# Performance work log

Hardware: AMD Instinct MI355X
Metric: run time of the kernel (lower is better)

## Reference

```python
import jax, jax.numpy as jnp
import numpy as np

RADIUS = 0.15
NSAMPLE = 128
NPOINT = 128
EPS = 1e-5  # BatchNorm eps (eval mode, running_mean=0, running_var=1)


def _bn(x, g, b):
    shape = (1, -1) + (1,) * (x.ndim - 2)
    return x * (g / jnp.sqrt(1.0 + EPS)).reshape(shape) + b.reshape(shape)


def _fps(x, npoint):
    # farthest point sampling; x: (Bk, N, 3) -> (Bk, npoint) int32
    Bn, N, _ = x.shape

    def step(carry, _):
        dist, far = carry
        c = jnp.take_along_axis(x, far[:, None, None], 1)  # (Bk,1,3)
        d = jnp.sum((x - c) ** 2, -1)
        dist = jnp.minimum(dist, d)
        return (dist, jnp.argmax(dist, -1).astype(jnp.int32)), far

    init = (jnp.full((Bn, N), 1e10, x.dtype), jnp.zeros((Bn,), jnp.int32))
    _, idxs = jax.lax.scan(step, init, None, length=npoint)
    return idxs.T  # (Bk, npoint)


def _sa_module(x, f, mlp):
    # PointnetSAModuleVotes: FPS -> ball query -> group (use_xyz, normalize_xyz)
    # -> shared MLP (conv2d 1x1 + BN + ReLU) -> max over nsample.
    Bk, M, _ = x.shape
    fps_idx = _fps(x, NPOINT)
    new_xyz = jnp.take_along_axis(x, fps_idx[..., None], 1)  # (Bk,np,3)
    d2 = jnp.sum((new_xyz[:, :, None, :] - x[:, None, :, :]) ** 2, -1)  # (Bk,np,M)
    cand = jnp.where(d2 < RADIUS ** 2, jnp.arange(M)[None, None, :], M)
    cand = jnp.sort(cand, -1)[..., :NSAMPLE]  # first nsample in-radius indices
    first = cand[..., :1]
    first = jnp.where(first == M, 0, first)
    idx = jnp.where(cand == M, first, cand)  # (Bk,np,ns), pad with first valid
    gx = jnp.take_along_axis(x, idx.reshape(Bk, -1)[..., None], 1).reshape(Bk, NPOINT, NSAMPLE, 3)
    gxn = (gx - new_xyz[:, :, None, :]) / RADIUS  # normalize_xyz=True
    gf = jnp.take_along_axis(f[:, :, None, :], idx[:, None, :, :], 3)  # (Bk,C,np,ns)
    h = jnp.concatenate([gxn.transpose(0, 3, 1, 2), gf], 1)  # (Bk, C+3, np, ns)
    for (w, b, g, be) in mlp:
        h = jax.nn.relu(_bn(jnp.einsum('oc,bcps->bops', w, h) + b[None, :, None, None], g, be))
    return new_xyz, h.max(-1)  # (Bk,np,3), (Bk,128,np)


def setup_inputs() -> dict:
    key = jax.random.key(0)
    ks = iter(jax.random.split(key, 40))
    B, M, K, C = 2, 1024, 19, 256
    inp = {}
    inp['xyz'] = jax.random.normal(next(ks), (B, M, K, 3), jnp.float32)
    inp['features'] = jax.random.normal(next(ks), (B, C, K, M), jnp.float32)

    def conv_p(prefix, cin, cout):
        inp[prefix + '_w'] = jax.random.normal(next(ks), (cout, cin), jnp.float32) * (1.0 / np.sqrt(cin))
        inp[prefix + '_b'] = jax.random.normal(next(ks), (cout,), jnp.float32) * 0.02
        inp[prefix + '_g'] = 1.0 + 0.1 * jax.random.normal(next(ks), (cout,), jnp.float32)
        inp[prefix + '_be'] = 0.02 * jax.random.normal(next(ks), (cout,), jnp.float32)

    conv_p('m1', C + 3, 128)  # use_xyz -> 259 in-channels
    conv_p('m2', 128, 128)
    conv_p('m3', 128, 128)
    conv_p('c1', 128, 128)
    conv_p('c2', 128, 128)
    inp['op_w'] = jax.random.normal(next(ks), (K, 5, 128), jnp.float32) * (1.0 / np.sqrt(128))
    inp['op_b'] = jax.random.normal(next(ks), (K, 5), jnp.float32) * 0.02
    return inp


def reference(xyz, features, m1_w, m1_b, m1_g, m1_be, m2_w, m2_b, m2_g, m2_be,
              m3_w, m3_b, m3_g, m3_be, c1_w, c1_b, c1_g, c1_be,
              c2_w, c2_b, c2_g, c2_be, op_w, op_b):
    B, M, K, _ = xyz.shape
    C = features.shape[1]
    # fold vote_factor k into the batch dim (all per-k SA/conv weights are shared)
    x = xyz.transpose(0, 2, 1, 3).reshape(B * K, M, 3)
    f = features.transpose(0, 2, 1, 3).reshape(B * K, C, M)
    mlp = [(m1_w, m1_b, m1_g, m1_be), (m2_w, m2_b, m2_g, m2_be), (m3_w, m3_b, m3_g, m3_be)]
    new_xyz, feat = _sa_module(x, f, mlp)
    net = jax.nn.relu(_bn(jnp.einsum('oc,bcp->bop', c1_w, feat) + c1_b[None, :, None], c1_g, c1_be))
    net = jax.nn.relu(_bn(jnp.einsum('oc,bcp->bop', c2_w, net) + c2_b[None, :, None], c2_g, c2_be))
    net = net.reshape(B, K, 128, NPOINT)
    # per-k output conv (conv_op ModuleList), 128 -> 2+3
    out = jnp.einsum('koc,bkcp->bkop', op_w, net) + op_b[None, :, :, None]
    net_t = out.transpose(0, 1, 3, 2)  # (B,K,np,5)
    agg_xyz = new_xyz.reshape(B, K, NPOINT, 3)
    center = agg_xyz + net_t[..., 2:5]  # decode_scores_
    scores = jnp.concatenate([net_t[..., :2], center], -1)  # obj(2) + center(3)
    return scores, agg_xyz, feat.reshape(B, K, 128, NPOINT)
```

## Files before the change

### kernel.cpp

```cpp
#include <hip/hip_runtime.h>
#include <math.h>

#define NBK   38

#define OFF_XC    0u
#define OFF_NXYZ  466944u
#define OFF_BIDX  525312u
#define OFF_W1F   3015680u
#define OFF_PREP  22938624u
#define OFF_WF    22955008u
#define OFF_CNT   23348224u

#define OUT_AGG   24320
#define OUT_FEAT  38912

typedef short bf16x8 __attribute__((ext_vector_type(8)));
typedef float f32x4  __attribute__((ext_vector_type(4)));
typedef int   v4i    __attribute__((ext_vector_type(4)));
typedef int   v2i    __attribute__((ext_vector_type(2)));

__device__ __forceinline__ float dist2f(float a0, float a1, float a2,
                                        float b0, float b1, float b2) {
#pragma clang fp contract(off)
  float d0 = a0 - b0;
  float d1 = a1 - b1;
  float d2 = a2 - b2;
  return d0 * d0 + d1 * d1 + d2 * d2;
}

__device__ __forceinline__ void split2rn(float v, unsigned& sh, unsigned& sm) {
  unsigned u = __float_as_uint(v);
  unsigned rh = (u + 0x7fffu + ((u >> 16) & 1u)) & 0xffff0000u;
  sh = rh >> 16;
  float r1 = v - __uint_as_float(rh);
  unsigned u1 = __float_as_uint(r1);
  unsigned rm = (u1 + 0x7fffu + ((u1 >> 16) & 1u)) & 0xffff0000u;
  sm = rm >> 16;
}

template<int CTRL, int RMASK>
__device__ __forceinline__ float fmax_dpp(float x) {
  int o = __builtin_amdgcn_update_dpp(__float_as_int(x), __float_as_int(x),
                                      CTRL, RMASK, 0xf, false);
  return fmaxf(x, __int_as_float(o));
}
template<int CTRL, int RMASK>
__device__ __forceinline__ unsigned umax_dpp(unsigned x) {
  unsigned o = (unsigned)__builtin_amdgcn_update_dpp((int)x, (int)x,
                                                     CTRL, RMASK, 0xf, false);
  return o > x ? o : x;
}
__device__ __forceinline__ float wave_fmax(float x) {
  x = fmax_dpp<0x111, 0xf>(x);
  x = fmax_dpp<0x112, 0xf>(x);
  x = fmax_dpp<0x114, 0xf>(x);
  x = fmax_dpp<0x118, 0xf>(x);
  x = fmax_dpp<0x142, 0xa>(x);
  x = fmax_dpp<0x143, 0xc>(x);
  return __int_as_float(__builtin_amdgcn_readlane(__float_as_int(x), 63));
}
__device__ __forceinline__ unsigned wave_umax(unsigned x) {
  x = umax_dpp<0x111, 0xf>(x);
  x = umax_dpp<0x112, 0xf>(x);
  x = umax_dpp<0x114, 0xf>(x);
  x = umax_dpp<0x118, 0xf>(x);
  x = umax_dpp<0x142, 0xa>(x);
  x = umax_dpp<0x143, 0xc>(x);
  return (unsigned)__builtin_amdgcn_readlane((int)x, 63);
}

__global__ __launch_bounds__(256, 2) void front_kernel(
    const float* __restrict__ xyz, const float* __restrict__ feats,
    const float* __restrict__ m1w, const float* __restrict__ m1b,
    const float* __restrict__ m1g, const float* __restrict__ m1be,
    const float* __restrict__ m2w, const float* __restrict__ m2b,
    const float* __restrict__ m2g, const float* __restrict__ m2be,
    const float* __restrict__ m3w, const float* __restrict__ m3b,
    const float* __restrict__ m3g, const float* __restrict__ m3be,
    const float* __restrict__ c1w, const float* __restrict__ c1b,
    const float* __restrict__ c1g, const float* __restrict__ c1be,
    const float* __restrict__ c2w, const float* __restrict__ c2b,
    const float* __restrict__ c2g, const float* __restrict__ c2be,
    float* __restrict__ xc, float* __restrict__ nxyz, float* __restrict__ agg,
    int* __restrict__ bidx, int* __restrict__ counts,
    float* __restrict__ W1f, short* __restrict__ Wf, float* __restrict__ prep)
{
  __shared__ __align__(16) char smem[32768];
  int bid = blockIdx.x, t = threadIdx.x;
  int wave = t >> 6, lane = t & 63;

  if (bid < NBK) {
    int bk = bid;
    int b = bk / 19, k = bk % 19;
    float* sx0 = (float*)smem;
    float* sx1 = sx0 + 1024;
    float* sx2 = sx1 + 1024;
    float* scen = sx2 + 1024;
    int* slot = (int*)(scen + 384);

    float x0[4], x1[4], x2[4], dist[4];
#pragma unroll
    for (int j = 0; j < 4; ++j) {
      int i = j * 256 + t;
      const float* src = xyz + ((size_t)((b * 1024 + i) * 19 + k)) * 3;
      x0[j] = src[0]; x1[j] = src[1]; x2[j] = src[2];
      sx0[i] = x0[j]; sx1[i] = x1[j]; sx2[i] = x2[j];
      xc[(bk * 3 + 0) * 1024 + i] = x0[j];
      xc[(bk * 3 + 1) * 1024 + i] = x1[j];
      xc[(bk * 3 + 2) * 1024 + i] = x2[j];
      dist[j] = 1e10f;
    }
    if (t == 0) {
#pragma unroll
      for (int w = 0; w < 4; ++w) {
        int* s = slot + w * 8;
        s[0] = 0; s[1] = 1023;
        s[2] = __float_as_int(x0[0]);
        s[3] = __float_as_int(x1[0]);
        s[4] = __float_as_int(x2[0]);
      }
    }
    __syncthreads();

    for (int it = 0; it < 128; ++it) {
      int pi = it & 1;
      const int* sl = slot + pi * 32;
      v4i s0 = *(const v4i*)(sl + 0);  int z0 = sl[4];
      v4i s1 = *(const v4i*)(sl + 8);  int z1 = sl[12];
      v4i s2 = *(const v4i*)(sl + 16); int z2 = sl[20];
      v4i s3 = *(const v4i*)(sl + 24); int z3 = sl[28];
      unsigned long long k0 = ((unsigned long long)(unsigned)s0.x << 32) | (unsigned)s0.y;
      unsigned long long k1 = ((unsigned long long)(unsigned)s1.x << 32) | (unsigned)s1.y;
      unsigned long long k2 = ((unsigned long long)(unsigned)s2.x << 32) | (unsigned)s2.y;
      unsigned long long k3 = ((unsigned long long)(unsigned)s3.x << 32) | (unsigned)s3.y;
      if (k1 > k0) { k0 = k1; s0 = s1; z0 = z1; }
      if (k3 > k2) { k2 = k3; s2 = s3; z2 = z3; }
      if (k2 > k0) { k0 = k2; s0 = s2; z0 = z2; }
      float c0 = __int_as_float(s0.z);
      float c1 = __int_as_float(s0.w);
      float c2 = __int_as_float(z0);
      if (t < 3) scen[it * 3 + t] = (t == 0) ? c0 : ((t == 1) ? c1 : c2);
      float dbest = -1.f; int ibest = 0;
#pragma unroll
      for (int j = 0; j < 4; ++j) {
        float d = dist2f(x0[j], x1[j], x2[j], c0, c1, c2);
        float dj = fminf(dist[j], d);
        dist[j] = dj;
        if (dj > dbest) { dbest = dj; ibest = j * 256 + t; }
      }
      float dmax = wave_fmax(dbest);
      unsigned cand = (dbest == dmax) ? (unsigned)(1023 - ibest) : 0u;
      unsigned key = wave_umax(cand);
      if (dbest == dmax && (unsigned)(1023 - ibest) == key) {
        int j = ibest >> 8;
        float wx = (j == 0) ? x0[0] : (j == 1) ? x0[1] : (j == 2) ? x0[2] : x0[3];
        float wy = (j == 0) ? x1[0] : (j == 1) ? x1[1] : (j == 2) ? x1[2] : x1[3];
        float wz = (j == 0) ? x2[0] : (j == 1) ? x2[1] : (j == 2) ? x2[2] : x2[3];
        int* s = slot + (pi ^ 1) * 32 + wave * 8;
        s[0] = __float_as_int(dmax);
        s[1] = (int)key;
        s[2] = __float_as_int(wx);
        s[3] = __float_as_int(wy);
        s[4] = __float_as_int(wz);
      }
      __syncthreads();
    }

    for (int e = t; e < 384; e += 256) {
      float v = scen[e];
      nxyz[bk * 384 + e] = v;
      agg[bk * 384 + e]  = v;
    }

    for (int p = wave * 32; p < wave * 32 + 32; ++p) {
      float c0 = scen[p * 3 + 0], c1 = scen[p * 3 + 1], c2 = scen[p * 3 + 2];
      int* outp = bidx + ((size_t)(bk * 128 + p)) * 128;
      int count = 0, first = 0;
      bool got = false;
      for (int ch = 0; ch < 16 && count < 128; ++ch) {
        int m = (ch << 6) + lane;
        float d = dist2f(sx0[m], sx1[m], sx2[m], c0, c1, c2);
        bool flag = d < 0.0225f;
        unsigned long long mask = __ballot(flag);
        if (!got && mask) { first = (ch << 6) + __builtin_ctzll(mask); got = true; }
        int pos = count + (int)__popcll(mask & ((1ull << lane) - 1ull));
        if (flag && pos < 128) outp[pos] = m;
        count += (int)__popcll(mask);
      }
      for (int j = count + lane; j < 128; j += 64) outp[j] = first;
      if (lane == 0) counts[bk * 128 + p] = count > 128 ? 128 : count;
    }
    return;
  }

  if (bid < 342) {
    short* ffrag = (short*)smem;
    int blk = bid - NBK;
    int bk = blk >> 3, m0 = (blk & 7) << 7;
    int b = bk / 19, k = bk % 19;
    int quad = lane >> 4, nl = lane & 15;
    int mloc = t & 127, chalf = t >> 7;
    int st_w = mloc >> 4, sl_w = mloc & 15;
    const float* fbase = feats + ((size_t)(b * 4864 + k)) * 1024 + m0 + mloc;
    const short* WA = Wf + 65536;

    f32x4 acc[2][8];
#pragma unroll
    for (int oi = 0; oi < 2; ++oi)
#pragma unroll
      for (int st = 0; st < 8; ++st) acc[oi][st] = (f32x4){0.f, 0.f, 0.f, 0.f};

    for (int ch = 0; ch < 4; ++ch) {
      int cbase = ch * 64 + chalf * 32;
#pragma unroll
      for (int g = 0; g < 4; ++g) {
        float v[8];
#pragma unroll
        for (int j = 0; j < 8; ++j)
          v[j] = fbase[(size_t)(cbase + g * 8 + j) * 19456];
        unsigned sh[8], sm[8];
#pragma unroll
        for (int j = 0; j < 8; ++j) split2rn(v[j], sh[j], sm[j]);
        int base = chalf * 4096 + st_w * 512 + (g * 16 + sl_w) * 8;
        v4i ph = {(int)(sh[0] | (sh[1] << 16)), (int)(sh[2] | (sh[3] << 16)),
                  (int)(sh[4] | (sh[5] << 16)), (int)(sh[6] | (sh[7] << 16))};
        *(v4i*)&ffrag[base] = ph;
        v4i pm = {(int)(sm[0] | (sm[1] << 16)), (int)(sm[2] | (sm[3] << 16)),
                  (int)(sm[4] | (sm[5] << 16)), (int)(sm[6] | (sm[7] << 16))};
        *(v4i*)&ffrag[base + 8192] = pm;
      }
      __syncthreads();
#pragma unroll
      for (int kkl = 0; kkl < 2; ++kkl) {
        int kk = ch * 2 + kkl;
        bf16x8 a[2][2];
#pragma unroll
        for (int oi = 0; oi < 2; ++oi) {
          int o_row = (wave * 2 + oi) * 16 + nl;
          const float* wsrc = m1w + o_row * 259 + 3 + kk * 32 + quad * 8;
          float wv[8];
#pragma unroll
          for (int j = 0; j < 8; ++j) wv[j] = wsrc[j];
          unsigned sh[8], sm[8];
#pragma unroll
          for (int j = 0; j < 8; ++j) split2rn(wv[j], sh[j], sm[j]);
          short ah[8], am[8];
#pragma unroll
          for (int j = 0; j < 8; ++j) { ah[j] = (short)sh[j]; am[j] = (short)sm[j]; }
          a[oi][0] = (bf16x8){ah[0], ah[1], ah[2], ah[3], ah[4], ah[5], ah[6], ah[7]};
          a[oi][1] = (bf16x8){am[0], am[1], am[2], am[3], am[4], am[5], am[6], am[7]};
        }
#pragma unroll
        for (int st = 0; st < 8; ++st) {
          const short* hb = ffrag + kkl * 4096 + st * 512 + lane * 8;
          bf16x8 b0 = *(const bf16x8*)hb;
          bf16x8 b1 = *(const bf16x8*)(hb + 8192);
#pragma unroll
          for (int oi = 0; oi < 2; ++oi) {
            f32x4 c = acc[oi][st];
            c = __builtin_amdgcn_mfma_f32_16x16x32_bf16(a[oi][1], b0, c, 0, 0, 0);
            c = __builtin_amdgcn_mfma_f32_16x16x32_bf16(a[oi][0], b1, c, 0, 0, 0);
            c = __builtin_amdgcn_mfma_f32_16x16x32_bf16(a[oi][0], b0, c, 0, 0, 0);
            acc[oi][st] = c;
          }
        }
      }
      __syncthreads();
    }
    (void)WA;
    float inv = 1.0f / sqrtf(1.0f + 1e-5f);
#pragma unroll
    for (int oi = 0; oi < 2; ++oi) {
      int o0 = (wave * 2 + oi) * 16 + quad * 4;
      float4 bb = *(const float4*)&m1b[o0];
      float4 gg = *(const float4*)&m1g[o0];
#pragma unroll
      for (int st = 0; st < 8; ++st) {
        int m_out = m0 + st * 16 + nl;
        f32x4 cc = acc[oi][st];
        float4 r;
        r.x = (cc[0] + bb.x) * (gg.x * inv);
        r.y = (cc[1] + bb.y) * (gg.y * inv);
        r.z = (cc[2] + bb.z) * (gg.z * inv);
        r.w = (cc[3] + bb.w) * (gg.w * inv);
        *(float4*)&W1f[((size_t)(bk * 1024 + m_out)) * 128 + o0] = r;
      }
    }
    return;
  }

  if (bid < 406) {
    int idx = (bid - 342) * 256 + t;
#pragma unroll
    for (int e = 0; e < 4; ++e) {
      int i = idx * 4 + e;
      if (i < 32768) {
        int c = i & 127, o = (i >> 7) & 127, l = i >> 14;
        float w = (l ? m3w : m2w)[o * 128 + c];
        unsigned sh, sm;
        split2rn(w, sh, sm);
        int ot = o >> 4, mm = o & 15, kk = c >> 5, q = (c & 31) >> 3, j = c & 7;
        int within = (q * 16 + mm) * 8 + j;
        Wf[(((l * 2 + 0) * 4 + kk) * 8 + ot) * 512 + within] = (short)sh;
        Wf[(((l * 2 + 1) * 4 + kk) * 8 + ot) * 512 + within] = (short)sm;
      } else {
        int jdx = i - 32768;
        int o = jdx >> 8, c = jdx & 255;
        float w = m1w[o * 259 + 3 + c];
        unsigned sh, sm;
        split2rn(w, sh, sm);
        int ot = o >> 4, mm = o & 15, kk = c >> 5, q = (c & 31) >> 3, j = c & 7;
        int within = (q * 16 + mm) * 8 + j;
        Wf[65536 + ((kk) * 8 + ot) * 512 + within] = (short)sh;
        Wf[65536 + ((8 + kk) * 8 + ot) * 512 + within] = (short)sm;
      }
    }
    return;
  }

  if (bid < 438) {
    int idx2 = (bid - 406) * 256 + t;
#pragma unroll
    for (int e = 0; e < 4; ++e) {
      int i = idx2 * 4 + e;
      int c = i & 127, o = (i >> 7) & 127, l = i >> 14;
      float w = (l ? c2w : c1w)[o * 128 + c];
      unsigned sh, sm;
      split2rn(w, sh, sm);
      int ot = o >> 4, mm = o & 15, kk = c >> 5, q = (c & 31) >> 3, j = c & 7;
      int within = (q * 16 + mm) * 8 + j;
      Wf[131072 + (((l * 2 + 0) * 4 + kk) * 8 + ot) * 512 + within] = (short)sh;
      Wf[131072 + (((l * 2 + 1) * 4 + kk) * 8 + ot) * 512 + within] = (short)sm;
    }
    return;
  }

  if (t < 128) {
    float inv = 1.0f / sqrtf(1.0f + 1e-5f);
    float a1 = m1g[t] * inv;
    prep[t] = a1;
    float a2 = m2g[t] * inv;  prep[256 + t] = a2;  prep[384 + t] = fmaf(m2b[t], a2, m2be[t]);
    float a3 = m3g[t] * inv;  prep[512 + t] = a3;  prep[640 + t] = fmaf(m3b[t], a3, m3be[t]);
    float ac1 = c1g[t] * inv; prep[768 + t] = ac1; prep[896 + t] = fmaf(c1b[t], ac1, c1be[t]);
    float ac2 = c2g[t] * inv; prep[1024 + t] = ac2; prep[1152 + t] = fmaf(c2b[t], ac2, c2be[t]);
    prep[1280 + 4 * t + 0] = m1w[t * 259 + 0] * a1;
    prep[1280 + 4 * t + 1] = m1w[t * 259 + 1] * a1;
    prep[1280 + 4 * t + 2] = m1w[t * 259 + 2] * a1;
    prep[1280 + 4 * t + 3] = m1be[t];
  }
}

__device__ __forceinline__ void mfma_layer(const short* __restrict__ Wf,
                                           const short* hfrag, int l,
                                           int wave, int lane, int nst_h,
                                           f32x4 acc[2][4])
{
#pragma unroll 1
  for (int kk = 0; kk < 4; ++kk) {
    bf16x8 a[2][2];
#pragma unroll
    for (int oi = 0; oi < 2; ++oi)
#pragma unroll
      for (int sp = 0; sp < 2; ++sp)
        a[oi][sp] = *(const bf16x8*)(Wf + (((l * 2 + sp) * 4 + kk) * 8 + (wave * 2 + oi)) * 512 + lane * 8);
    for (int st = 0; st < nst_h; ++st) {
      const short* hb = hfrag + kk * 2048 + st * 512 + lane * 8;
      bf16x8 b0 = *(const bf16x8*)(hb);
      bf16x8 b1 = *(const bf16x8*)(hb + 8192);
#pragma unroll
      for (int oi = 0; oi < 2; ++oi) {
        f32x4 c = acc[oi][st];
        c = __builtin_amdgcn_mfma_f32_16x16x32_bf16(a[oi][1], b0, c, 0, 0, 0);
        c = __builtin_amdgcn_mfma_f32_16x16x32_bf16(a[oi][0], b1, c, 0, 0, 0);
        c = __builtin_amdgcn_mfma_f32_16x16x32_bf16(a[oi][0], b0, c, 0, 0, 0);
        acc[oi][st] = c;
      }
    }
  }
}

__global__ __launch_bounds__(256, 3) void sa_kernel(
    const float* __restrict__ xc, const float* __restrict__ nxyz,
    const int* __restrict__ bidx, const int* __restrict__ counts,
    const float* __restrict__ W1f, const float* __restrict__ prep,
    const short* __restrict__ Wf, float* __restrict__ feat_out)
{
  __shared__ __align__(16) short hfrag[16384];
  __shared__ float pcs[512];
  __shared__ float sm[32 * 128];
  __shared__ float ccen[12];
  __shared__ int scnt[4];
  int gb = blockIdx.x, bk = gb >> 5, pb = (gb & 31) << 2;
  int t = threadIdx.x;
  int wave = t >> 6, lane = t & 63;
  int quad = lane >> 4, nl = lane & 15;

  pcs[t] = prep[1280 + t];
  pcs[256 + t] = prep[1536 + t];
  if (t < 4) scnt[t] = counts[bk * 128 + pb + t];
  if (t < 12) {
    int bb = t / 3, c = t % 3;
    ccen[t] = nxyz[(bk * 128 + pb + bb) * 3 + c];
  }
  __syncthreads();
  int n0 = (scnt[0] + 15) >> 4, n1 = (scnt[1] + 15) >> 4;
  int n2 = (scnt[2] + 15) >> 4, n3 = (scnt[3] + 15) >> 4;
  int pf1 = n0, pf2 = n0 + n1, pf3 = n0 + n1 + n2, T = n0 + n1 + n2 + n3;

  for (int q0 = 0; q0 < T; q0 += 4) {
    int nst_h = T - q0;
    if (nst_h > 4) nst_h = 4;
    {
      int cg = wave;
      int st = lane >> 4, sl = lane & 15;
      if (st < nst_h) {
        int q = q0 + st;
        int bq = (q >= pf1) + (q >= pf2) + (q >= pf3);
        int tstart = (bq == 0) ? 0 : (bq == 1) ? pf1 : (bq == 2) ? pf2 : pf3;
        int tslot = q - tstart;
        int m = bidx[((size_t)(bk * 128 + pb + bq)) * 128 + tslot * 16 + sl];
        float cen0 = ccen[bq * 3 + 0], cen1 = ccen[bq * 3 + 1], cen2 = ccen[bq * 3 + 2];
        float g0 = (xc[(bk * 3 + 0) * 1024 + m] - cen0) * (1.0f / 0.15f);
        float g1 = (xc[(bk * 3 + 1) * 1024 + m] - cen1) * (1.0f / 0.15f);
        float g2 = (xc[(bk * 3 + 2) * 1024 + m] - cen2) * (1.0f / 0.15f);
        const float4* wrow = (const float4*)(W1f + ((size_t)(bk * 1024 + m)) * 128 + cg * 32);
        const float4* pcp = (const float4*)pcs + cg * 32;
#pragma unroll
        for (int g = 0; g < 4; ++g) {
          float4 wva = wrow[g * 2], wvb = wrow[g * 2 + 1];
          float wv[8] = {wva.x, wva.y, wva.z, wva.w, wvb.x, wvb.y, wvb.z, wvb.w};
          unsigned sh[8], smv[8];
#pragma unroll
          for (int e = 0; e < 8; ++e) {
            float4 pc = pcp[g * 8 + e];
            float hv = fmaxf(wv[e] + pc.x * g0 + pc.y * g1 + pc.z * g2 + pc.w, 0.f);
            split2rn(hv, sh[e], smv[e]);
          }
          int base = (cg * 4 + st) * 512 + (g * 16 + sl) * 8;
          v4i ph = {(int)(sh[0] | (sh[1] << 16)), (int)(sh[2] | (sh[3] << 16)),
                    (int)(sh[4] | (sh[5] << 16)), (int)(sh[6] | (sh[7] << 16))};
          *(v4i*)&hfrag[base] = ph;
          v4i pm = {(int)(smv[0] | (smv[1] << 16)), (int)(smv[2] | (smv[3] << 16)),
                    (int)(smv[4] | (smv[5] << 16)), (int)(smv[6] | (smv[7] << 16))};
          *(v4i*)&hfrag[base + 8192] = pm;
        }
      }
    }
    __syncthreads();

    f32x4 acc[2][4];
#pragma unroll
    for (int oi = 0; oi < 2; ++oi)
#pragma unroll
      for (int st = 0; st < 4; ++st) acc[oi][st] = (f32x4){0.f, 0.f, 0.f, 0.f};
    mfma_layer(Wf, hfrag, 0, wave, lane, nst_h, acc);
    __syncthreads();

#pragma unroll
    for (int oi = 0; oi < 2; ++oi) {
      int o0 = (wave * 2 + oi) * 16 + quad * 4;
      float4 al = *(const float4*)&prep[256 + o0];
      float4 be = *(const float4*)&prep[384 + o0];
      int kk2 = o0 >> 5, g2 = (o0 & 31) >> 3, j0 = o0 & 7;
      for (int st = 0; st < nst_h; ++st) {
        f32x4 cc = acc[oi][st];
        float v0 = fmaxf(fmaf(cc[0], al.x, be.x), 0.f);
        float v1 = fmaxf(fmaf(cc[1], al.y, be.y), 0.f);
        float v2 = fmaxf(fmaf(cc[2], al.z, be.z), 0.f);
        float v3 = fmaxf(fmaf(cc[3], al.w, be.w), 0.f);
        unsigned h0, m0_, h1, m1_, h2, m2_, h3, m3_;
        split2rn(v0, h0, m0_); split2rn(v1, h1, m1_);
        split2rn(v2, h2, m2_); split2rn(v3, h3, m3_);
        int base = (kk2 * 4 + st) * 512 + (g2 * 16 + nl) * 8 + j0;
        v2i w0 = {(int)(h0 | (h1 << 16)), (int)(h2 | (h3 << 16))};
        *(v2i*)&hfrag[base] = w0;
        v2i w1 = {(int)(m0_ | (m1_ << 16)), (int)(m2_ | (m3_ << 16))};
        *(v2i*)&hfrag[base + 8192] = w1;
      }
    }
    __syncthreads();

#pragma unroll
    for (int oi = 0; oi < 2; ++oi)
#pragma unroll
      for (int st = 0; st < 4; ++st) acc[oi][st] = (f32x4){0.f, 0.f, 0.f, 0.f};
    mfma_layer(Wf, hfrag, 1, wave, lane, nst_h, acc);

#pragma unroll
    for (int oi = 0; oi < 2; ++oi) {
      int o0 = (wave * 2 + oi) * 16 + quad * 4;
      float4 al = *(const float4*)&prep[512 + o0];
      float4 be = *(const float4*)&prep[640 + o0];
      for (int st = 0; st < nst_h; ++st) {
        f32x4 cc = acc[oi][st];
        float v[4];
        v[0] = fmaxf(fmaf(cc[0], al.x, be.x), 0.f);
        v[1] = fmaxf(fmaf(cc[1], al.y, be.y), 0.f);
        v[2] = fmaxf(fmaf(cc[2], al.z, be.z), 0.f);
        v[3] = fmaxf(fmaf(cc[3], al.w, be.w), 0.f);
#pragma unroll
        for (int r = 0; r < 4; ++r) {
          float x = v[r];
          x = fmaxf(x, __shfl_xor(x, 1));
          x = fmaxf(x, __shfl_xor(x, 2));
          x = fmaxf(x, __shfl_xor(x, 4));
          x = fmaxf(x, __shfl_xor(x, 8));
          if (nl == 0) sm[(q0 + st) * 128 + o0 + r] = x;
        }
      }
    }
    __syncthreads();
  }

#pragma unroll
  for (int e = t; e < 512; e += 256) {
    int bb = e >> 7, o = e & 127;
    int qs = (bb == 0) ? 0 : (bb == 1) ? pf1 : (bb == 2) ? pf2 : pf3;
    int nq = (bb == 0) ? n0 : (bb == 1) ? n1 : (bb == 2) ? n2 : n3;
    float v = sm[qs * 128 + o];
    for (int q = 1; q < nq; ++q) v = fmaxf(v, sm[(qs + q) * 128 + o]);
    feat_out[(((size_t)bk) << 14) + (o << 7) + pb + bb] = v;
  }
}

__global__ __launch_bounds__(256) void head_kernel(const float* __restrict__ featg,
    const float* __restrict__ prep, const short* __restrict__ Wf,
    const float* __restrict__ nxyz, const float* __restrict__ opw,
    const float* __restrict__ opb, float* __restrict__ scores)
{
  __shared__ __align__(16) short hfrag[16384];
  __shared__ float hplain[128 * 65];
  int bk = blockIdx.x >> 1, p0 = (blockIdx.x & 1) << 6;
  int t = threadIdx.x;
  int wave = t >> 6, lane = t & 63;
  int quad = lane >> 4, nl = lane & 15;
  const short* WC = Wf + 131072;

  {
    int cg = wave;
    int st = lane >> 4, sl = lane & 15;
    const float* fb = featg + (bk << 14) + p0 + lane;
#pragma unroll
    for (int g = 0; g < 4; ++g) {
      float v[8];
#pragma unroll
      for (int e = 0; e < 8; ++e)
        v[e] = fb[(cg * 32 + g * 8 + e) << 7];
      unsigned sh[8], sm[8];
#pragma unroll
      for (int e = 0; e < 8; ++e) split2rn(v[e], sh[e], sm[e]);
      int base = (cg * 4 + st) * 512 + (g * 16 + sl) * 8;
      v4i ph = {(int)(sh[0] | (sh[1] << 16)), (int)(sh[2] | (sh[3] << 16)),
                (int)(sh[4] | (sh[5] << 16)), (int)(sh[6] | (sh[7] << 16))};
      *(v4i*)&hfrag[base] = ph;
      v4i pm = {(int)(sm[0] | (sm[1] << 16)), (int)(sm[2] | (sm[3] << 16)),
                (int)(sm[4] | (sm[5] << 16)), (int)(sm[6] | (sm[7] << 16))};
      *(v4i*)&hfrag[base + 8192] = pm;
    }
  }
  __syncthreads();

  f32x4 acc[2][4];
#pragma unroll
  for (int oi = 0; oi < 2; ++oi)
#pragma unroll
    for (int st = 0; st < 4; ++st) acc[oi][st] = (f32x4){0.f, 0.f, 0.f, 0.f};
  mfma_layer(WC, hfrag, 0, wave, lane, 4, acc);
  __syncthreads();

#pragma unroll
  for (int oi = 0; oi < 2; ++oi) {
    int o0 = (wave * 2 + oi) * 16 + quad * 4;
    float4 al = *(const float4*)&prep[768 + o0];
    float4 be = *(const float4*)&prep[896 + o0];
    int kk2 = o0 >> 5, g2 = (o0 & 31) >> 3, j0 = o0 & 7;
#pragma unroll
    for (int st = 0; st < 4; ++st) {
      f32x4 cc = acc[oi][st];
      float v0 = fmaxf(fmaf(cc[0], al.x, be.x), 0.f);
      float v1 = fmaxf(fmaf(cc[1], al.y, be.y), 0.f);
      float v2 = fmaxf(fmaf(cc[2], al.z, be.z), 0.f);
      float v3 = fmaxf(fmaf(cc[3], al.w, be.w), 0.f);
      unsigned h0, m0_, h1, m1_, h2, m2_, h3, m3_;
      split2rn(v0, h0, m0_); split2rn(v1, h1, m1_);
      split2rn(v2, h2, m2_); split2rn(v3, h3, m3_);
      int base = (kk2 * 4 + st) * 512 + (g2 * 16 + nl) * 8 + j0;
      v2i w0 = {(int)(h0 | (h1 << 16)), (int)(h2 | (h3 << 16))};
      *(v2i*)&hfrag[base] = w0;
      v2i w1 = {(int)(m0_ | (m1_ << 16)), (int)(m2_ | (m3_ << 16))};
      *(v2i*)&hfrag[base + 8192] = w1;
    }
  }
  __syncthreads();

#pragma unroll
  for (int oi = 0; oi < 2; ++oi)
#pragma unroll
    for (int st = 0; st < 4; ++st) acc[oi][st] = (f32x4){0.f, 0.f, 0.f, 0.f};
  mfma_layer(WC, hfrag, 1, wave, lane, 4, acc);

#pragma unroll
  for (int oi = 0; oi < 2; ++oi) {
    int o0 = (wave * 2 + oi) * 16 + quad * 4;
    float4 al = *(const float4*)&prep[1024 + o0];
    float4 be = *(const float4*)&prep[1152 + o0];
#pragma unroll
    for (int st = 0; st < 4; ++st) {
      f32x4 cc = acc[oi][st];
      int p = st * 16 + nl;
      hplain[(o0 + 0) * 65 + p] = fmaxf(fmaf(cc[0], al.x, be.x), 0.f);
      hplain[(o0 + 1) * 65 + p] = fmaxf(fmaf(cc[1], al.y, be.y), 0.f);
      hplain[(o0 + 2) * 65 + p] = fmaxf(fmaf(cc[2], al.z, be.z), 0.f);
      hplain[(o0 + 3) * 65 + p] = fmaxf(fmaf(cc[3], al.w, be.w), 0.f);
    }
  }
  __syncthreads();

  if (t < 64) {
    int p = t, k = bk % 19;
    float res[5];
#pragma unroll
    for (int j = 0; j < 5; ++j) {
      const float* wr = opw + ((size_t)(k * 5 + j)) * 128;
      float a = opb[k * 5 + j];
      for (int c = 0; c < 128; ++c) a = fmaf(wr[c], hplain[c * 65 + p], a);
      res[j] = a;
    }
    int pg = p0 + p;
    float a0 = nxyz[(bk * 128 + pg) * 3 + 0];
    float a1 = nxyz[(bk * 128 + pg) * 3 + 1];
    float a2 = nxyz[(bk * 128 + pg) * 3 + 2];
    float* sc = scores + ((size_t)(bk * 128 + pg)) * 5;
    sc[0] = res[0];
    sc[1] = res[1];
    sc[2] = a0 + res[2];
    sc[3] = a1 + res[3];
    sc[4] = a2 + res[4];
  }
}

extern "C" void kernel_launch(void* const* d_in, const int* in_sizes, int n_in,
                              void* d_out, int out_size, void* d_ws, size_t ws_size,
                              hipStream_t stream) {
  (void)in_sizes; (void)n_in; (void)out_size; (void)ws_size;
  const float* xyz  = (const float*)d_in[0];
  const float* fts  = (const float*)d_in[1];
  const float* m1w  = (const float*)d_in[2];
  const float* m1b  = (const float*)d_in[3];
  const float* m1g  = (const float*)d_in[4];
  const float* m1be = (const float*)d_in[5];
  const float* m2w  = (const float*)d_in[6];
  const float* m2b  = (const float*)d_in[7];
  const float* m2g  = (const float*)d_in[8];
  const float* m2be = (const float*)d_in[9];
  const float* m3w  = (const float*)d_in[10];
  const float* m3b  = (const float*)d_in[11];
  const float* m3g  = (const float*)d_in[12];
  const float* m3be = (const float*)d_in[13];
  const float* c1w  = (const float*)d_in[14];
  const float* c1b  = (const float*)d_in[15];
  const float* c1g  = (const float*)d_in[16];
  const float* c1be = (const float*)d_in[17];
  const float* c2w  = (const float*)d_in[18];
  const float* c2b  = (const float*)d_in[19];
  const float* c2g  = (const float*)d_in[20];
  const float* c2be = (const float*)d_in[21];
  const float* opw  = (const float*)d_in[22];
  const float* opb  = (const float*)d_in[23];

  float* out = (float*)d_out;
  char* ws = (char*)d_ws;
  float* xc   = (float*)(ws + OFF_XC);
  float* nxyz = (float*)(ws + OFF_NXYZ);
  int*   bidx = (int*)(ws + OFF_BIDX);
  float* W1f  = (float*)(ws + OFF_W1F);
  float* prep = (float*)(ws + OFF_PREP);
  short* Wf   = (short*)(ws + OFF_WF);
  int*   cnt  = (int*)(ws + OFF_CNT);

  hipLaunchKernelGGL(front_kernel, dim3(439), dim3(256), 0, stream,
                     xyz, fts, m1w, m1b, m1g, m1be, m2w, m2b, m2g, m2be,
                     m3w, m3b, m3g, m3be, c1w, c1b, c1g, c1be,
                     c2w, c2b, c2g, c2be,
                     xc, nxyz, out + OUT_AGG, bidx, cnt, W1f, Wf, prep);
  hipLaunchKernelGGL(sa_kernel, dim3(NBK * 32), dim3(256), 0, stream,
                     xc, nxyz, bidx, cnt, W1f, prep, Wf, out + OUT_FEAT);
  hipLaunchKernelGGL(head_kernel, dim3(NBK * 2), dim3(256), 0, stream,
                     out + OUT_FEAT, prep, Wf, nxyz, opw, opb, out);
}
```

Before: 333.0 us.

## Widen front kernel to 1024 threads with one point per thread in FPS

The front kernel now launches 1024-thread blocks. In farthest point sampling each thread owns one point instead of four. The per-iteration argmax becomes a shuffle wave reduction followed by a 16-wave reduction in shared memory, which needs two barriers per step. Ball query spreads 8 centers per wave across 16 waves. The weight-split blocks are merged into fewer larger blocks, and the unused m1w fragment prep is dropped. The MFMA blocks simply park their extra 768 threads at the barriers. The wider launch bound can cut the register budget of the MFMA path, and the extra barrier lengthens the serial FPS loop.

```diff
diff --git a/kernel.cpp b/kernel.cpp
--- a/kernel.cpp
+++ b/kernel.cpp
@@ -38,38 +38,7 @@
   sm = rm >> 16;
 }
 
-template<int CTRL, int RMASK>
-__device__ __forceinline__ float fmax_dpp(float x) {
-  int o = __builtin_amdgcn_update_dpp(__float_as_int(x), __float_as_int(x),
-                                      CTRL, RMASK, 0xf, false);
-  return fmaxf(x, __int_as_float(o));
-}
-template<int CTRL, int RMASK>
-__device__ __forceinline__ unsigned umax_dpp(unsigned x) {
-  unsigned o = (unsigned)__builtin_amdgcn_update_dpp((int)x, (int)x,
-                                                     CTRL, RMASK, 0xf, false);
-  return o > x ? o : x;
-}
-__device__ __forceinline__ float wave_fmax(float x) {
-  x = fmax_dpp<0x111, 0xf>(x);
-  x = fmax_dpp<0x112, 0xf>(x);
-  x = fmax_dpp<0x114, 0xf>(x);
-  x = fmax_dpp<0x118, 0xf>(x);
-  x = fmax_dpp<0x142, 0xa>(x);
-  x = fmax_dpp<0x143, 0xc>(x);
-  return __int_as_float(__builtin_amdgcn_readlane(__float_as_int(x), 63));
-}
-__device__ __forceinline__ unsigned wave_umax(unsigned x) {
-  x = umax_dpp<0x111, 0xf>(x);
-  x = umax_dpp<0x112, 0xf>(x);
-  x = umax_dpp<0x114, 0xf>(x);
-  x = umax_dpp<0x118, 0xf>(x);
-  x = umax_dpp<0x142, 0xa>(x);
-  x = umax_dpp<0x143, 0xc>(x);
-  return (unsigned)__builtin_amdgcn_readlane((int)x, 63);
-}
-
-__global__ __launch_bounds__(256, 2) void front_kernel(
+__global__ __launch_bounds__(1024, 4) void front_kernel(
     const float* __restrict__ xyz, const float* __restrict__ feats,
     const float* __restrict__ m1w, const float* __restrict__ m1b,
     const float* __restrict__ m1g, const float* __restrict__ m1be,
@@ -96,83 +65,60 @@
     float* sx1 = sx0 + 1024;
     float* sx2 = sx1 + 1024;
     float* scen = sx2 + 1024;
-    int* slot = (int*)(scen + 384);
-
-    float x0[4], x1[4], x2[4], dist[4];
-#pragma unroll
-    for (int j = 0; j < 4; ++j) {
-      int i = j * 256 + t;
-      const float* src = xyz + ((size_t)((b * 1024 + i) * 19 + k)) * 3;
-      x0[j] = src[0]; x1[j] = src[1]; x2[j] = src[2];
-      sx0[i] = x0[j]; sx1[i] = x1[j]; sx2[i] = x2[j];
-      xc[(bk * 3 + 0) * 1024 + i] = x0[j];
-      xc[(bk * 3 + 1) * 1024 + i] = x1[j];
-      xc[(bk * 3 + 2) * 1024 + i] = x2[j];
-      dist[j] = 1e10f;
-    }
-    if (t == 0) {
-#pragma unroll
-      for (int w = 0; w < 4; ++w) {
-        int* s = slot + w * 8;
-        s[0] = 0; s[1] = 1023;
-        s[2] = __float_as_int(x0[0]);
-        s[3] = __float_as_int(x1[0]);
-        s[4] = __float_as_int(x2[0]);
-      }
-    }
+    float* sd = scen + 384;
+    int* si = (int*)(sd + 16);
+    int* sfar = si + 16;
+
+    const float* src = xyz + ((size_t)((b * 1024 + t) * 19 + k)) * 3;
+    float x0 = src[0], x1 = src[1], x2 = src[2];
+    sx0[t] = x0; sx1[t] = x1; sx2[t] = x2;
+    xc[(bk * 3 + 0) * 1024 + t] = x0;
+    xc[(bk * 3 + 1) * 1024 + t] = x1;
+    xc[(bk * 3 + 2) * 1024 + t] = x2;
+    if (t == 0) *sfar = 0;
+    float dist = 1e10f;
     __syncthreads();
 
     for (int it = 0; it < 128; ++it) {
-      int pi = it & 1;
-      const int* sl = slot + pi * 32;
-      v4i s0 = *(const v4i*)(sl + 0);  int z0 = sl[4];
-      v4i s1 = *(const v4i*)(sl + 8);  int z1 = sl[12];
-      v4i s2 = *(const v4i*)(sl + 16); int z2 = sl[20];
-      v4i s3 = *(const v4i*)(sl + 24); int z3 = sl[28];
-      unsigned long long k0 = ((unsigned long long)(unsigned)s0.x << 32) | (unsigned)s0.y;
-      unsigned long long k1 = ((unsigned long long)(unsigned)s1.x << 32) | (unsigned)s1.y;
-      unsigned long long k2 = ((unsigned long long)(unsigned)s2.x << 32) | (unsigned)s2.y;
-      unsigned long long k3 = ((unsigned long long)(unsigned)s3.x << 32) | (unsigned)s3.y;
-      if (k1 > k0) { k0 = k1; s0 = s1; z0 = z1; }
-      if (k3 > k2) { k2 = k3; s2 = s3; z2 = z3; }
-      if (k2 > k0) { k0 = k2; s0 = s2; z0 = z2; }
-      float c0 = __int_as_float(s0.z);
-      float c1 = __int_as_float(s0.w);
-      float c2 = __int_as_float(z0);
+      int far = *sfar;
+      float c0 = sx0[far], c1 = sx1[far], c2 = sx2[far];
       if (t < 3) scen[it * 3 + t] = (t == 0) ? c0 : ((t == 1) ? c1 : c2);
-      float dbest = -1.f; int ibest = 0;
-#pragma unroll
-      for (int j = 0; j < 4; ++j) {
-        float d = dist2f(x0[j], x1[j], x2[j], c0, c1, c2);
-        float dj = fminf(dist[j], d);
-        dist[j] = dj;
-        if (dj > dbest) { dbest = dj; ibest = j * 256 + t; }
-      }
-      float dmax = wave_fmax(dbest);
-      unsigned cand = (dbest == dmax) ? (unsigned)(1023 - ibest) : 0u;
-      unsigned key = wave_umax(cand);
-      if (dbest == dmax && (unsigned)(1023 - ibest) == key) {
-        int j = ibest >> 8;
-        float wx = (j == 0) ? x0[0] : (j == 1) ? x0[1] : (j == 2) ? x0[2] : x0[3];
-        float wy = (j == 0) ? x1[0] : (j == 1) ? x1[1] : (j == 2) ? x1[2] : x1[3];
-        float wz = (j == 0) ? x2[0] : (j == 1) ? x2[1] : (j == 2) ? x2[2] : x2[3];
-        int* s = slot + (pi ^ 1) * 32 + wave * 8;
-        s[0] = __float_as_int(dmax);
-        s[1] = (int)key;
-        s[2] = __float_as_int(wx);
-        s[3] = __float_as_int(wy);
-        s[4] = __float_as_int(wz);
+      float d = dist2f(x0, x1, x2, c0, c1, c2);
+      dist = fminf(dist, d);
+      float dmax = dist;
+#pragma unroll
+      for (int off = 1; off <= 32; off <<= 1)
+        dmax = fmaxf(dmax, __shfl_xor(dmax, off));
+      unsigned long long mk = __ballot(dist == dmax);
+      if (lane == 0) {
+        sd[wave] = dmax;
+        si[wave] = (wave << 6) + __builtin_ctzll(mk);
       }
       __syncthreads();
-    }
-
-    for (int e = t; e < 384; e += 256) {
-      float v = scen[e];
-      nxyz[bk * 384 + e] = v;
-      agg[bk * 384 + e]  = v;
-    }
-
-    for (int p = wave * 32; p < wave * 32 + 32; ++p) {
+      if (t < 16) {
+        float dw = sd[t]; int iw = si[t];
+        unsigned long long key =
+            ((unsigned long long)__float_as_uint(dw) << 32) | (unsigned)(1023 - iw);
+#pragma unroll
+        for (int off = 8; off >= 1; off >>= 1) {
+          unsigned hi = (unsigned)(key >> 32), lo = (unsigned)key;
+          unsigned h2 = __shfl_xor(hi, off);
+          unsigned l2 = __shfl_xor(lo, off);
+          unsigned long long ok = ((unsigned long long)h2 << 32) | l2;
+          if (ok > key) key = ok;
+        }
+        if (t == 0) *sfar = 1023 - (int)(key & 0xffffffffu);
+      }
+      __syncthreads();
+    }
+
+    if (t < 384) {
+      float v = scen[t];
+      nxyz[bk * 384 + t] = v;
+      agg[bk * 384 + t]  = v;
+    }
+
+    for (int p = wave * 8; p < wave * 8 + 8; ++p) {
       float c0 = scen[p * 3 + 0], c1 = scen[p * 3 + 1], c2 = scen[p * 3 + 2];
       int* outp = bidx + ((size_t)(bk * 128 + p)) * 128;
       int count = 0, first = 0;
@@ -195,6 +141,10 @@
 
   if (bid < 342) {
     short* ffrag = (short*)smem;
+    if (t >= 256) {
+      for (int i = 0; i < 8; ++i) __syncthreads();
+      return;
+    }
     int blk = bid - NBK;
     int bk = blk >> 3, m0 = (blk & 7) << 7;
     int b = bk / 19, k = bk % 19;
@@ -202,7 +152,6 @@
     int mloc = t & 127, chalf = t >> 7;
     int st_w = mloc >> 4, sl_w = mloc & 15;
     const float* fbase = feats + ((size_t)(b * 4864 + k)) * 1024 + m0 + mloc;
-    const short* WA = Wf + 65536;
 
     f32x4 acc[2][8];
 #pragma unroll
@@ -267,7 +216,6 @@
       }
       __syncthreads();
     }
-    (void)WA;
     float inv = 1.0f / sqrtf(1.0f + 1e-5f);
 #pragma unroll
     for (int oi = 0; oi < 2; ++oi) {
@@ -289,37 +237,25 @@
     return;
   }
 
-  if (bid < 406) {
-    int idx = (bid - 342) * 256 + t;
+  if (bid < 350) {
+    int idx = (bid - 342) * 1024 + t;
 #pragma unroll
     for (int e = 0; e < 4; ++e) {
       int i = idx * 4 + e;
-      if (i < 32768) {
-        int c = i & 127, o = (i >> 7) & 127, l = i >> 14;
-        float w = (l ? m3w : m2w)[o * 128 + c];
-        unsigned sh, sm;
-        split2rn(w, sh, sm);
-        int ot = o >> 4, mm = o & 15, kk = c >> 5, q = (c & 31) >> 3, j = c & 7;
-        int within = (q * 16 + mm) * 8 + j;
-        Wf[(((l * 2 + 0) * 4 + kk) * 8 + ot) * 512 + within] = (short)sh;
-        Wf[(((l * 2 + 1) * 4 + kk) * 8 + ot) * 512 + within] = (short)sm;
-      } else {
-        int jdx = i - 32768;
-        int o = jdx >> 8, c = jdx & 255;
-        float w = m1w[o * 259 + 3 + c];
-        unsigned sh, sm;
-        split2rn(w, sh, sm);
-        int ot = o >> 4, mm = o & 15, kk = c >> 5, q = (c & 31) >> 3, j = c & 7;
-        int within = (q * 16 + mm) * 8 + j;
-        Wf[65536 + ((kk) * 8 + ot) * 512 + within] = (short)sh;
-        Wf[65536 + ((8 + kk) * 8 + ot) * 512 + within] = (short)sm;
-      }
+      int c = i & 127, o = (i >> 7) & 127, l = i >> 14;
+      float w = (l ? m3w : m2w)[o * 128 + c];
+      unsigned sh, sm;
+      split2rn(w, sh, sm);
+      int ot = o >> 4, mm = o & 15, kk = c >> 5, q = (c & 31) >> 3, j = c & 7;
+      int within = (q * 16 + mm) * 8 + j;
+      Wf[(((l * 2 + 0) * 4 + kk) * 8 + ot) * 512 + within] = (short)sh;
+      Wf[(((l * 2 + 1) * 4 + kk) * 8 + ot) * 512 + within] = (short)sm;
     }
     return;
   }
 
-  if (bid < 438) {
-    int idx2 = (bid - 406) * 256 + t;
+  if (bid < 358) {
+    int idx2 = (bid - 350) * 1024 + t;
 #pragma unroll
     for (int e = 0; e < 4; ++e) {
       int i = idx2 * 4 + e;
@@ -678,7 +614,7 @@
   short* Wf   = (short*)(ws + OFF_WF);
   int*   cnt  = (int*)(ws + OFF_CNT);
 
-  hipLaunchKernelGGL(front_kernel, dim3(439), dim3(256), 0, stream,
+  hipLaunchKernelGGL(front_kernel, dim3(359), dim3(1024), 0, stream,
                      xyz, fts, m1w, m1b, m1g, m1be, m2w, m2b, m2g, m2be,
                      m3w, m3b, m3g, m3be, c1w, c1b, c1g, c1be,
                      c2w, c2b, c2g, c2be,
```

New measurement: 302.4 us. -9.2%, faster.
